# Performance work log

Measured on AMD Instinct MI355X. Metric: run time of the kernel, lower is better.

## Reference

```python
import jax, jax.numpy as jnp
import numpy as np

SIZE = 256
K_SIGN = 100000.0
EPS = 1e-05

# mesh: torch.meshgrid default indexing='ij', stacked, flattened, / size -> (size^2, 2)
_MESH = jnp.stack(jnp.meshgrid(jnp.arange(SIZE, dtype=jnp.float32),
                               jnp.arange(SIZE, dtype=jnp.float32),
                               indexing='ij'), axis=-1).reshape(-1, 2) / SIZE


def setup_inputs() -> dict:
    key = jax.random.key(0)
    # contour values must lie in [0, 1]
    contour = jax.random.uniform(key, (2, 2, 64, 2), dtype=jnp.float32)
    return {"contour": contour}


def reference(contour) -> jnp.ndarray:
    b, n, k, _ = contour.shape
    c = contour.reshape(b * n, 1, k, 2)          # (bn, 1, K, 2)
    mesh = _MESH[None, :, None, :]               # (1, S^2, 1, 2)
    diff = c - mesh                              # (bn, S^2, K, 2)

    norm_diff = jnp.linalg.norm(diff, axis=-1)   # (bn, S^2, K)
    min_diff = jnp.min(norm_diff, axis=2).reshape(b * n, SIZE, SIZE)

    roll_diff = jnp.roll(diff, -1, axis=2)       # next vertex along K
    # torch: sign = (diff * roll(roll_diff,1,dims=3)); sign[...,1]-sign[...,0]
    #       = diff_y*roll_x - diff_x*roll_y
    cross = diff[..., 1] * roll_diff[..., 0] - diff[..., 0] * roll_diff[..., 1]
    sign = jnp.tanh(K_SIGN * cross)

    nd = jnp.clip(norm_diff, EPS)
    nr = jnp.clip(jnp.linalg.norm(roll_diff, axis=-1), EPS)
    scalar_product = jnp.sum(diff * roll_diff, axis=-1)
    cos_ang = jnp.clip(scalar_product / (nd * nr), -1.0 + EPS, 1.0 - EPS)
    angles = jnp.arccos(cos_ang)

    winding = jnp.abs(jnp.sum(sign * angles, axis=2)) / (2.0 * jnp.pi)  # (bn, S^2)
    resize = winding.reshape(b * n, SIZE, SIZE)

    prod = resize * min_diff
    dmap = prod / jnp.max(prod)                  # global max normalization
    return dmap.reshape(b, n, SIZE, SIZE)
```

## Files before the change

kernel.cpp:

```cpp
#include <hip/hip_runtime.h>
#include <math.h>

#define SZ 256
#define KPTS 64
#define GROUPS 4
#define SEGS_PER (KPTS / GROUPS)
#define NBLK (4 * SZ * GROUPS)
#define K_SIGN 100000.0f
#define EPS_C 1e-5f
#define INV_2PI 0.15915494309189535f
#define PI_F 3.14159265358979323846f
#define K2_LOG2E 288539.00817779269f

__device__ __forceinline__ float fast_rcp(float x)  { return __builtin_amdgcn_rcpf(x); }
__device__ __forceinline__ float fast_sqrt(float x) { return __builtin_amdgcn_sqrtf(x); }
__device__ __forceinline__ float fast_rsq(float x)  { return __builtin_amdgcn_rsqf(x); }
__device__ __forceinline__ float fast_exp2(float x) { return __builtin_amdgcn_exp2f(x); }

__device__ __forceinline__ float fast_tanh_k(float cross) {
    float t = fast_exp2(K2_LOG2E * cross);
    return fmaf(-2.0f, fast_rcp(t + 1.0f), 1.0f);
}

__device__ __forceinline__ float fast_acos(float x) {
    float ax = fabsf(x);
    float s  = fast_sqrt(1.0f - ax);
    float p  = s * fmaf(ax, fmaf(ax, fmaf(ax, -0.0187292994f, 0.0742610037f),
                                  -0.2121143937f), 1.5707288f);
    return (x >= 0.0f) ? p : (PI_F - p);
}


__global__ __launch_bounds__(256) void contour_prod_kernel(
    const float* __restrict__ contour,
    float* __restrict__ out,
    float* __restrict__ ws)
{
    __shared__ float cx[KPTS + 1];
    __shared__ float cy[KPTS + 1];
    __shared__ float wred[4];

    const int blk = blockIdx.x;
    const int jq  = blk & 3;
    const int i   = (blk >> 2) & 255;
    const int bn  = blk >> 10;

    const int t = threadIdx.x;
    if (t < KPTS) {
        float x = contour[(bn * KPTS + t) * 2 + 0];
        float y = contour[(bn * KPTS + t) * 2 + 1];
        cx[t] = x; cy[t] = y;
        if (t == 0) { cx[KPTS] = x; cy[KPTS] = y; }
    }
    __syncthreads();

    const int g    = t & 3;
    const int jloc = t >> 2;
    const int j    = (jq << 6) + jloc;

    const float mx = (float)i * (1.0f / (float)SZ);
    const float my = (float)j * (1.0f / (float)SZ);

    const int base = g * SEGS_PER;

    float dxc   = cx[base] - mx;
    float dyc   = cy[base] - my;
    float n2c   = fmaf(dxc, dxc, dyc * dyc);
    float invc  = fast_rsq(n2c);
    float minn2 = n2c;
    float acc   = 0.0f;

    #pragma unroll
    for (int kk = 0; kk < SEGS_PER; ++kk) {
        const float dxn  = cx[base + kk + 1] - mx;
        const float dyn  = cy[base + kk + 1] - my;
        const float n2n  = fmaf(dxn, dxn, dyn * dyn);
        const float invn = fast_rsq(n2n);
        minn2 = fminf(minn2, n2n);

        const float cross = dyc * dxn - dxc * dyn;
        const float sgn   = fast_tanh_k(cross);

        const float dot = fmaf(dxc, dxn, dyc * dyn);
        float cosang = dot * invc * invn;
        cosang = fminf(fmaxf(cosang, -1.0f + EPS_C), 1.0f - EPS_C);
        const float ang = fast_acos(cosang);

        acc = fmaf(sgn, ang, acc);

        dxc = dxn; dyc = dyn; invc = invn;
    }

    acc += __shfl_xor(acc, 1, 64);
    acc += __shfl_xor(acc, 2, 64);
    minn2 = fminf(minn2, __shfl_xor(minn2, 1, 64));
    minn2 = fminf(minn2, __shfl_xor(minn2, 2, 64));

    const float prod = fabsf(acc) * INV_2PI * fast_sqrt(minn2);
    if (g == 0)
        out[((bn << 8) + i) * SZ + j] = prod;

    float wmax = prod;
    #pragma unroll
    for (int off = 32; off > 0; off >>= 1)
        wmax = fmaxf(wmax, __shfl_down(wmax, off, 64));
    if ((t & 63) == 0) wred[t >> 6] = wmax;
    __syncthreads();
    if (t == 0)
        ws[blk] = fmaxf(fmaxf(wred[0], wred[1]), fmaxf(wred[2], wred[3]));
}

__global__ __launch_bounds__(256) void contour_norm_kernel(
    float4* __restrict__ out,
    const float* __restrict__ ws)
{
    __shared__ float wred[4];
    __shared__ float smax;

    const int t = threadIdx.x;
    const float4* w4 = (const float4*)ws;

    float m = 0.0f;
    #pragma unroll
    for (int r = 0; r < 4; ++r) {
        float4 v = w4[t + (r << 8)];
        m = fmaxf(m, fmaxf(fmaxf(v.x, v.y), fmaxf(v.z, v.w)));
    }
    #pragma unroll
    for (int off = 32; off > 0; off >>= 1)
        m = fmaxf(m, __shfl_down(m, off, 64));
    if ((t & 63) == 0) wred[t >> 6] = m;
    __syncthreads();
    if (t == 0)
        smax = fmaxf(fmaxf(wred[0], wred[1]), fmaxf(wred[2], wred[3]));
    __syncthreads();

    const float inv = 1.0f / smax;
    const int idx = blockIdx.x * 256 + t;
    float4 v = out[idx];
    v.x *= inv; v.y *= inv; v.z *= inv; v.w *= inv;
    out[idx] = v;
}

extern "C" void kernel_launch(void* const* d_in, const int* in_sizes, int n_in,
                              void* d_out, int out_size, void* d_ws, size_t ws_size,
                              hipStream_t stream)
{
    const float* contour = (const float*)d_in[0];
    float* out = (float*)d_out;
    float* ws  = (float*)d_ws;

    contour_prod_kernel<<<NBLK, SZ, 0, stream>>>(contour, out, ws);
    contour_norm_kernel<<<out_size / 4 / 256, 256, 0, stream>>>((float4*)out, ws);
}
```

Baseline: 23.87 us.

## Compute two adjacent pixels per thread and halve block count

Each thread now handles two neighbouring mesh columns that share the same x offset. This lets it reuse dx, dx², dxc·dxn and the shared-memory contour loads across both pixels. The contour is stored as float2, one rsq of the product n2c·n2n replaces the separate per-vertex rsq, and outputs are written as float2. The grid shrinks to 2048 blocks and the norm kernel reads half as many partial maxima. The cost is more registers per thread and fewer waves to hide latency.

```diff
diff --git a/kernel.cpp b/kernel.cpp
--- a/kernel.cpp
+++ b/kernel.cpp
@@ -5,7 +5,7 @@
 #define KPTS 64
 #define GROUPS 4
 #define SEGS_PER (KPTS / GROUPS)
-#define NBLK (4 * SZ * GROUPS)
+#define NBLK (4 * SZ * 2)
 #define K_SIGN 100000.0f
 #define EPS_C 1e-5f
 #define INV_2PI 0.15915494309189535f
@@ -36,71 +36,95 @@
     float* __restrict__ out,
     float* __restrict__ ws)
 {
-    __shared__ float cx[KPTS + 1];
-    __shared__ float cy[KPTS + 1];
+    __shared__ float2 cpt[KPTS + 1];
     __shared__ float wred[4];
 
     const int blk = blockIdx.x;
-    const int jq  = blk & 3;
-    const int i   = (blk >> 2) & 255;
-    const int bn  = blk >> 10;
+    const int jq  = blk & 1;
+    const int i   = (blk >> 1) & 255;
+    const int bn  = blk >> 9;
 
     const int t = threadIdx.x;
     if (t < KPTS) {
-        float x = contour[(bn * KPTS + t) * 2 + 0];
-        float y = contour[(bn * KPTS + t) * 2 + 1];
-        cx[t] = x; cy[t] = y;
-        if (t == 0) { cx[KPTS] = x; cy[KPTS] = y; }
+        float2 p = ((const float2*)contour)[bn * KPTS + t];
+        cpt[t] = p;
+        if (t == 0) cpt[KPTS] = p;
     }
     __syncthreads();
 
     const int g    = t & 3;
-    const int jloc = t >> 2;
-    const int j    = (jq << 6) + jloc;
+    const int slot = t >> 2;
+    const int j0   = (jq << 7) + (slot << 1);
 
-    const float mx = (float)i * (1.0f / (float)SZ);
-    const float my = (float)j * (1.0f / (float)SZ);
+    const float mx  = (float)i  * (1.0f / (float)SZ);
+    const float my0 = (float)j0 * (1.0f / (float)SZ);
+    const float my1 = my0 + (1.0f / (float)SZ);
 
     const int base = g * SEGS_PER;
 
-    float dxc   = cx[base] - mx;
-    float dyc   = cy[base] - my;
-    float n2c   = fmaf(dxc, dxc, dyc * dyc);
-    float invc  = fast_rsq(n2c);
-    float minn2 = n2c;
-    float acc   = 0.0f;
+    float2 cp = cpt[base];
+    float dxc  = cp.x - mx;
+    float dyc0 = cp.y - my0;
+    float dyc1 = cp.y - my1;
+    const float dx2c = dxc * dxc;
+    float n2c0 = fmaf(dyc0, dyc0, dx2c);
+    float n2c1 = fmaf(dyc1, dyc1, dx2c);
+    float mn0  = n2c0, mn1 = n2c1;
+    float acc0 = 0.0f, acc1 = 0.0f;
 
     #pragma unroll
     for (int kk = 0; kk < SEGS_PER; ++kk) {
-        const float dxn  = cx[base + kk + 1] - mx;
-        const float dyn  = cy[base + kk + 1] - my;
-        const float n2n  = fmaf(dxn, dxn, dyn * dyn);
-        const float invn = fast_rsq(n2n);
-        minn2 = fminf(minn2, n2n);
+        const float2 cn = cpt[base + kk + 1];
+        const float dxn  = cn.x - mx;
+        const float dyn0 = cn.y - my0;
+        const float dyn1 = cn.y - my1;
+        const float dx2  = dxn * dxn;
+        const float n2n0 = fmaf(dyn0, dyn0, dx2);
+        const float n2n1 = fmaf(dyn1, dyn1, dx2);
+        mn0 = fminf(mn0, n2n0);
+        mn1 = fminf(mn1, n2n1);
 
-        const float cross = dyc * dxn - dxc * dyn;
-        const float sgn   = fast_tanh_k(cross);
+        const float dd = dxc * dxn;
+        const float cross0 = fmaf(dyc0, dxn, -dxc * dyn0);
+        const float cross1 = fmaf(dyc1, dxn, -dxc * dyn1);
+        const float dot0   = fmaf(dyc0, dyn0, dd);
+        const float dot1   = fmaf(dyc1, dyn1, dd);
 
-        const float dot = fmaf(dxc, dxn, dyc * dyn);
-        float cosang = dot * invc * invn;
-        cosang = fminf(fmaxf(cosang, -1.0f + EPS_C), 1.0f - EPS_C);
-        const float ang = fast_acos(cosang);
+        float ca0 = dot0 * fast_rsq(n2c0 * n2n0);
+        float ca1 = dot1 * fast_rsq(n2c1 * n2n1);
+        ca0 = fminf(fmaxf(ca0, -1.0f + EPS_C), 1.0f - EPS_C);
+        ca1 = fminf(fmaxf(ca1, -1.0f + EPS_C), 1.0f - EPS_C);
+        const float ang0 = fast_acos(ca0);
+        const float ang1 = fast_acos(ca1);
 
-        acc = fmaf(sgn, ang, acc);
+        const float s0 = fast_tanh_k(cross0);
+        const float s1 = fast_tanh_k(cross1);
 
-        dxc = dxn; dyc = dyn; invc = invn;
+        acc0 = fmaf(s0, ang0, acc0);
+        acc1 = fmaf(s1, ang1, acc1);
+
+        dxc = dxn;
+        dyc0 = dyn0; dyc1 = dyn1;
+        n2c0 = n2n0; n2c1 = n2n1;
     }
 
-    acc += __shfl_xor(acc, 1, 64);
-    acc += __shfl_xor(acc, 2, 64);
-    minn2 = fminf(minn2, __shfl_xor(minn2, 1, 64));
-    minn2 = fminf(minn2, __shfl_xor(minn2, 2, 64));
+    acc0 += __shfl_xor(acc0, 1, 64);
+    acc0 += __shfl_xor(acc0, 2, 64);
+    acc1 += __shfl_xor(acc1, 1, 64);
+    acc1 += __shfl_xor(acc1, 2, 64);
+    mn0 = fminf(mn0, __shfl_xor(mn0, 1, 64));
+    mn0 = fminf(mn0, __shfl_xor(mn0, 2, 64));
+    mn1 = fminf(mn1, __shfl_xor(mn1, 1, 64));
+    mn1 = fminf(mn1, __shfl_xor(mn1, 2, 64));
 
-    const float prod = fabsf(acc) * INV_2PI * fast_sqrt(minn2);
-    if (g == 0)
-        out[((bn << 8) + i) * SZ + j] = prod;
+    const float prod0 = fabsf(acc0) * INV_2PI * fast_sqrt(mn0);
+    const float prod1 = fabsf(acc1) * INV_2PI * fast_sqrt(mn1);
+    if (g == 0) {
+        float2 pv = make_float2(prod0, prod1);
+        ((float2*)out)[(((bn << 8) + i) << 7) + (jq << 6) + slot] = pv;
+    }
 
-    float wmax = prod;
+    float wmax = fmaxf(prod0, prod1);
     #pragma unroll
     for (int off = 32; off > 0; off >>= 1)
         wmax = fmaxf(wmax, __shfl_down(wmax, off, 64));
@@ -121,10 +145,11 @@
     const float4* w4 = (const float4*)ws;
 
     float m = 0.0f;
-    #pragma unroll
-    for (int r = 0; r < 4; ++r) {
-        float4 v = w4[t + (r << 8)];
-        m = fmaxf(m, fmaxf(fmaxf(v.x, v.y), fmaxf(v.z, v.w)));
+    {
+        float4 a = w4[t];
+        float4 b = w4[t + 256];
+        m = fmaxf(fmaxf(fmaxf(a.x, a.y), fmaxf(a.z, a.w)),
+                  fmaxf(fmaxf(b.x, b.y), fmaxf(b.z, b.w)));
     }
     #pragma unroll
     for (int off = 32; off > 0; off >>= 1)
```

Result: faster. 21.94 us (-8.1%).

## Compute four pixels per thread to reuse x-terms and cut block count

Applied to the files above, without the earlier changes.

Each thread now evaluates four adjacent j pixels, so the x-dependent work (dx, dx², dx product) is shared across them. One rsq on the product of squared norms replaces two per-segment rsq calls. The grid shrinks fourfold and the output is written as float4, which also reduces the partial-max buffer the norm kernel reads. The cost is more registers per thread (launch bounds now request 4 blocks) and fewer blocks to spread across CUs.

```diff
diff --git a/kernel.cpp b/kernel.cpp
--- a/kernel.cpp
+++ b/kernel.cpp
@@ -5,7 +5,8 @@
 #define KPTS 64
 #define GROUPS 4
 #define SEGS_PER (KPTS / GROUPS)
-#define NBLK (4 * SZ * GROUPS)
+#define PX 4
+#define NBLK (4 * SZ)
 #define K_SIGN 100000.0f
 #define EPS_C 1e-5f
 #define INV_2PI 0.15915494309189535f
@@ -31,76 +32,100 @@
 }
 
 
-__global__ __launch_bounds__(256) void contour_prod_kernel(
+__global__ __launch_bounds__(256, 4) void contour_prod_kernel(
     const float* __restrict__ contour,
     float* __restrict__ out,
     float* __restrict__ ws)
 {
-    __shared__ float cx[KPTS + 1];
-    __shared__ float cy[KPTS + 1];
+    __shared__ float2 cpt[KPTS + 1];
     __shared__ float wred[4];
 
     const int blk = blockIdx.x;
-    const int jq  = blk & 3;
-    const int i   = (blk >> 2) & 255;
-    const int bn  = blk >> 10;
+    const int i   = blk & 255;
+    const int bn  = blk >> 8;
 
     const int t = threadIdx.x;
     if (t < KPTS) {
-        float x = contour[(bn * KPTS + t) * 2 + 0];
-        float y = contour[(bn * KPTS + t) * 2 + 1];
-        cx[t] = x; cy[t] = y;
-        if (t == 0) { cx[KPTS] = x; cy[KPTS] = y; }
+        float2 p = ((const float2*)contour)[bn * KPTS + t];
+        cpt[t] = p;
+        if (t == 0) cpt[KPTS] = p;
     }
     __syncthreads();
 
     const int g    = t & 3;
-    const int jloc = t >> 2;
-    const int j    = (jq << 6) + jloc;
+    const int slot = t >> 2;
+    const int j0   = slot << 2;
 
-    const float mx = (float)i * (1.0f / (float)SZ);
-    const float my = (float)j * (1.0f / (float)SZ);
+    const float mx  = (float)i  * (1.0f / (float)SZ);
+    float my[PX];
+    #pragma unroll
+    for (int q = 0; q < PX; ++q)
+        my[q] = (float)(j0 + q) * (1.0f / (float)SZ);
 
     const int base = g * SEGS_PER;
 
-    float dxc   = cx[base] - mx;
-    float dyc   = cy[base] - my;
-    float n2c   = fmaf(dxc, dxc, dyc * dyc);
-    float invc  = fast_rsq(n2c);
-    float minn2 = n2c;
-    float acc   = 0.0f;
+    float2 cp = cpt[base];
+    float dxc = cp.x - mx;
+    const float dx2c = dxc * dxc;
+    float dyc[PX], mn[PX], acc[PX];
+    #pragma unroll
+    for (int q = 0; q < PX; ++q) {
+        dyc[q] = cp.y - my[q];
+        mn[q]  = fmaf(dyc[q], dyc[q], dx2c);
+        acc[q] = 0.0f;
+    }
+    float n2c[PX];
+    #pragma unroll
+    for (int q = 0; q < PX; ++q) n2c[q] = mn[q];
 
     #pragma unroll
     for (int kk = 0; kk < SEGS_PER; ++kk) {
-        const float dxn  = cx[base + kk + 1] - mx;
-        const float dyn  = cy[base + kk + 1] - my;
-        const float n2n  = fmaf(dxn, dxn, dyn * dyn);
-        const float invn = fast_rsq(n2n);
-        minn2 = fminf(minn2, n2n);
+        const float2 cn = cpt[base + kk + 1];
+        const float dxn = cn.x - mx;
+        const float dx2 = dxn * dxn;
+        const float dd  = dxc * dxn;
 
-        const float cross = dyc * dxn - dxc * dyn;
-        const float sgn   = fast_tanh_k(cross);
+        #pragma unroll
+        for (int q = 0; q < PX; ++q) {
+            const float dyn  = cn.y - my[q];
+            const float n2n  = fmaf(dyn, dyn, dx2);
+            mn[q] = fminf(mn[q], n2n);
 
-        const float dot = fmaf(dxc, dxn, dyc * dyn);
-        float cosang = dot * invc * invn;
-        cosang = fminf(fmaxf(cosang, -1.0f + EPS_C), 1.0f - EPS_C);
-        const float ang = fast_acos(cosang);
+            const float cross = fmaf(dyc[q], dxn, -dxc * dyn);
+            const float dot   = fmaf(dyc[q], dyn, dd);
 
-        acc = fmaf(sgn, ang, acc);
+            float cosang = dot * fast_rsq(n2c[q] * n2n);
+            cosang = fminf(fmaxf(cosang, -1.0f + EPS_C), 1.0f - EPS_C);
+            const float ang = fast_acos(cosang);
+            const float sgn = fast_tanh_k(cross);
 
-        dxc = dxn; dyc = dyn; invc = invn;
+            acc[q] = fmaf(sgn, ang, acc[q]);
+
+            dyc[q] = dyn;
+            n2c[q] = n2n;
+        }
+        dxc = dxn;
     }
 
-    acc += __shfl_xor(acc, 1, 64);
-    acc += __shfl_xor(acc, 2, 64);
-    minn2 = fminf(minn2, __shfl_xor(minn2, 1, 64));
-    minn2 = fminf(minn2, __shfl_xor(minn2, 2, 64));
+    #pragma unroll
+    for (int q = 0; q < PX; ++q) {
+        acc[q] += __shfl_xor(acc[q], 1, 64);
+        acc[q] += __shfl_xor(acc[q], 2, 64);
+        mn[q] = fminf(mn[q], __shfl_xor(mn[q], 1, 64));
+        mn[q] = fminf(mn[q], __shfl_xor(mn[q], 2, 64));
+    }
 
-    const float prod = fabsf(acc) * INV_2PI * fast_sqrt(minn2);
-    if (g == 0)
-        out[((bn << 8) + i) * SZ + j] = prod;
+    float prod[PX];
+    #pragma unroll
+    for (int q = 0; q < PX; ++q)
+        prod[q] = fabsf(acc[q]) * INV_2PI * fast_sqrt(mn[q]);
 
-    float wmax = prod;
+    if (g == 0) {
+        ((float4*)out)[((bn << 8) + i) * (SZ / 4) + slot] =
+            make_float4(prod[0], prod[1], prod[2], prod[3]);
+    }
+
+    float wmax = fmaxf(fmaxf(prod[0], prod[1]), fmaxf(prod[2], prod[3]));
     #pragma unroll
     for (int off = 32; off > 0; off >>= 1)
         wmax = fmaxf(wmax, __shfl_down(wmax, off, 64));
@@ -120,12 +145,8 @@
     const int t = threadIdx.x;
     const float4* w4 = (const float4*)ws;
 
-    float m = 0.0f;
-    #pragma unroll
-    for (int r = 0; r < 4; ++r) {
-        float4 v = w4[t + (r << 8)];
-        m = fmaxf(m, fmaxf(fmaxf(v.x, v.y), fmaxf(v.z, v.w)));
-    }
+    float4 v0 = w4[t];
+    float m = fmaxf(fmaxf(v0.x, v0.y), fmaxf(v0.z, v0.w));
     #pragma unroll
     for (int off = 32; off > 0; off >>= 1)
         m = fmaxf(m, __shfl_down(m, off, 64));
```

Measured after the change: 21.14 us. -11.5%, faster.
